# Performance work log

Measured on AMD Instinct MI355X. Metric: run time of the kernel, lower is better.

The kernel has to match this reference:

```python
import jax, jax.numpy as jnp
from jax import lax
import numpy as np


def _dilate3x3(img):
    # Faithful to torch: zero-pad by 1 (f.pad default), then 3x3 max over the
    # padded window (strel of ones => plain max, zeros from padding included).
    imgp = jnp.pad(img, ((0, 0), (0, 0), (1, 1), (1, 1)))
    return lax.reduce_window(imgp, -jnp.inf, lax.max,
                             (1, 1, 3, 3), (1, 1, 1, 1), 'VALID')


def setup_inputs() -> dict:
    key = jax.random.key(0)
    x = jax.random.normal(key, (32, 3, 512, 512), dtype=jnp.float32)
    return {"in_tensor": x, "n_pixels": 20}


def reference(in_tensor, n_pixels):
    # smoother = linspace(1, 0, n+1); smoother_diff = -diff => 1/n per step (linear)
    smoother = jnp.linspace(1.0, 0.0, n_pixels + 1)
    sdiff = (-jnp.diff(smoother)).astype(in_tensor.dtype)  # [n_pixels]

    def step(carry, w):
        out, img = carry
        out = out + w * img
        img = _dilate3x3(img)
        return (out, img), None

    init = (jnp.zeros_like(in_tensor), in_tensor)
    (out, _), _ = lax.scan(step, init, sdiff)
    return out
```

## Files before the change

### kernel.cpp

```cpp
#include <hip/hip_runtime.h>

#define IMG_W 512
#define IMG_H 512
#define TILE 88
#define HALO 20
#define NSTEP 19
#define RH 8
#define RW 8
#define REG 128

__device__ __forceinline__ float max3f(float a, float b, float c) {
    return fmaxf(fmaxf(a, b), c);
}

__device__ __forceinline__ float dpp_shr1(float v) {
    int i = __builtin_bit_cast(int, v);
    i = __builtin_amdgcn_update_dpp(0, i, 0x111, 0xf, 0xf, true);
    return __builtin_bit_cast(float, i);
}
__device__ __forceinline__ float dpp_shl1(float v) {
    int i = __builtin_bit_cast(int, v);
    i = __builtin_amdgcn_update_dpp(0, i, 0x101, 0xf, 0xf, true);
    return __builtin_bit_cast(float, i);
}

__device__ __forceinline__ void hrow(const float (&Ar)[RW], float (&h)[RW]) {
    float hl = dpp_shr1(Ar[RW - 1]);
    float hr = dpp_shl1(Ar[0]);
    h[0] = max3f(hl, Ar[0], Ar[1]);
    #pragma unroll
    for (int c = 1; c < RW - 1; ++c) h[c] = max3f(Ar[c - 1], Ar[c], Ar[c + 1]);
    h[RW - 1] = max3f(Ar[RW - 2], Ar[RW - 1], hr);
}

template<bool XM, bool YM>
__device__ __forceinline__ void rowop(const float (&hm1)[RW], const float (&hc)[RW],
                                      const float (&hn)[RW], float (&Ar)[RW],
                                      float (&accr)[RW], const float (&colm)[RW],
                                      float rm, bool needR) {
    float v[RW];
    #pragma unroll
    for (int c = 0; c < RW; ++c) v[c] = max3f(hm1[c], hc[c], hn[c]);
    if (XM) {
        #pragma unroll
        for (int c = 0; c < RW; ++c) v[c] *= colm[c];
    }
    if (YM) {
        if (needR) {
            #pragma unroll
            for (int c = 0; c < RW; ++c) v[c] *= rm;
        }
    }
    #pragma unroll
    for (int c = 0; c < RW; ++c) { Ar[c] = v[c]; accr[c] += v[c]; }
}

template<bool XM, bool YM>
__device__ __forceinline__ void body(const float* __restrict__ xc, float* __restrict__ oc,
                                     int gx0, int gy0, int tx, int ty,
                                     float4 (*topH4)[2][16][16], float4 (*botH4)[2][16][16]) {
    const int rx = tx * RW;
    const int ry = ty * RH;
    const int gx = gx0 + rx;
    const int gy = gy0 + ry;

    float A[RH][RW];
    float acc[RH][RW];
    float colm[RW], rowm[RH];
    bool needR = false;

    if (XM) {
        #pragma unroll
        for (int c = 0; c < RW; ++c) {
            int xx = gx + c;
            colm[c] = (xx >= 0 && xx < IMG_W) ? 1.f : 0.f;
        }
    }
    if (YM) {
        #pragma unroll
        for (int r = 0; r < RH; ++r) {
            int yy = gy + r;
            rowm[r] = (yy >= 0 && yy < IMG_H) ? 1.f : 0.f;
        }
        needR = (gy < 0) || (gy + RH > IMG_H);
    }

    if (XM || YM) {
        const bool fullin = (gx >= 0) && (gx + RW <= IMG_W) && (gy >= 0) && (gy + RH <= IMG_H);
        if (fullin) {
            #pragma unroll
            for (int r = 0; r < RH; ++r) {
                const float4* rp = (const float4*)(xc + (size_t)(gy + r) * IMG_W + gx);
                float4 v0 = rp[0], v1 = rp[1];
                A[r][0] = v0.x; A[r][1] = v0.y; A[r][2] = v0.z; A[r][3] = v0.w;
                A[r][4] = v1.x; A[r][5] = v1.y; A[r][6] = v1.z; A[r][7] = v1.w;
            }
        } else {
            #pragma unroll
            for (int r = 0; r < RH; ++r) {
                const int yr = gy + r;
                const int yy = min(max(yr, 0), IMG_H - 1);
                float rmv = (yr >= 0 && yr < IMG_H) ? 1.f : 0.f;
                const float* rp = xc + (size_t)yy * IMG_W;
                #pragma unroll
                for (int c = 0; c < RW; ++c) {
                    const int xr = gx + c;
                    const int xx = min(max(xr, 0), IMG_W - 1);
                    float m = rmv;
                    if (XM) m *= colm[c];
                    A[r][c] = rp[xx] * m;
                }
            }
        }
    } else {
        #pragma unroll
        for (int r = 0; r < RH; ++r) {
            const float4* rp = (const float4*)(xc + (size_t)(gy + r) * IMG_W + gx);
            float4 v0 = rp[0], v1 = rp[1];
            A[r][0] = v0.x; A[r][1] = v0.y; A[r][2] = v0.z; A[r][3] = v0.w;
            A[r][4] = v1.x; A[r][5] = v1.y; A[r][6] = v1.z; A[r][7] = v1.w;
        }
    }
    #pragma unroll
    for (int r = 0; r < RH; ++r) {
        #pragma unroll
        for (int c = 0; c < RW; ++c) acc[r][c] = A[r][c];
    }

    #pragma unroll 1
    for (int s = 0; s < NSTEP; ++s) {
        const int buf = s & 1;
        float hc[RW], h7[RW];
        hrow(A[0], hc);
        hrow(A[RH - 1], h7);
        topH4[buf][0][ty][tx] = make_float4(hc[0], hc[1], hc[2], hc[3]);
        topH4[buf][1][ty][tx] = make_float4(hc[4], hc[5], hc[6], hc[7]);
        botH4[buf][0][ty][tx] = make_float4(h7[0], h7[1], h7[2], h7[3]);
        botH4[buf][1][ty][tx] = make_float4(h7[4], h7[5], h7[6], h7[7]);
        __syncthreads();
        const int tyu = ty > 0  ? ty - 1 : 0;
        const int tyd = ty < 15 ? ty + 1 : 15;
        float hm1[RW], hbot[RW];
        {
            float4 u0 = botH4[buf][0][tyu][tx], u1 = botH4[buf][1][tyu][tx];
            float4 d0 = topH4[buf][0][tyd][tx], d1 = topH4[buf][1][tyd][tx];
            hm1[0] = u0.x; hm1[1] = u0.y; hm1[2] = u0.z; hm1[3] = u0.w;
            hm1[4] = u1.x; hm1[5] = u1.y; hm1[6] = u1.z; hm1[7] = u1.w;
            hbot[0] = d0.x; hbot[1] = d0.y; hbot[2] = d0.z; hbot[3] = d0.w;
            hbot[4] = d1.x; hbot[5] = d1.y; hbot[6] = d1.z; hbot[7] = d1.w;
        }
        #pragma unroll
        for (int r = 0; r < RH; ++r) {
            float hn[RW];
            if (r < RH - 2) {
                hrow(A[r + 1], hn);
            } else if (r == RH - 2) {
                #pragma unroll
                for (int c = 0; c < RW; ++c) hn[c] = h7[c];
            } else {
                #pragma unroll
                for (int c = 0; c < RW; ++c) hn[c] = hbot[c];
            }
            rowop<XM, YM>(hm1, hc, hn, A[r], acc[r], colm, YM ? rowm[r] : 1.f, needR);
            #pragma unroll
            for (int c = 0; c < RW; ++c) { hm1[c] = hc[c]; hc[c] = hn[c]; }
        }
    }

    if (XM || YM) {
        #pragma unroll
        for (int r = 0; r < RH; ++r) {
            const int rr = ry + r;
            const int yy = gy0 + rr;
            if (rr >= HALO && rr < HALO + TILE && yy < IMG_H) {
                #pragma unroll
                for (int c = 0; c < RW; ++c) {
                    const int cc = rx + c;
                    const int xx = gx0 + cc;
                    if (cc >= HALO && cc < HALO + TILE && xx < IMG_W)
                        oc[(size_t)yy * IMG_W + xx] = 0.05f * acc[r][c];
                }
            }
        }
    } else {
        #pragma unroll
        for (int r = 0; r < RH; ++r) {
            const int rr = ry + r;
            if (rr < HALO || rr >= HALO + TILE) continue;
            const int yy = gy0 + rr;
            float* rowp = oc + (size_t)yy * IMG_W + gx;
            if (tx >= 3 && tx <= 12) {
                ((float4*)rowp)[0] = make_float4(0.05f * acc[r][0], 0.05f * acc[r][1],
                                                 0.05f * acc[r][2], 0.05f * acc[r][3]);
                ((float4*)rowp)[1] = make_float4(0.05f * acc[r][4], 0.05f * acc[r][5],
                                                 0.05f * acc[r][6], 0.05f * acc[r][7]);
            } else if (tx == 2) {
                ((float4*)rowp)[1] = make_float4(0.05f * acc[r][4], 0.05f * acc[r][5],
                                                 0.05f * acc[r][6], 0.05f * acc[r][7]);
            } else if (tx == 13) {
                ((float4*)rowp)[0] = make_float4(0.05f * acc[r][0], 0.05f * acc[r][1],
                                                 0.05f * acc[r][2], 0.05f * acc[r][3]);
            }
        }
    }
}

__global__ __launch_bounds__(256, 2)
void blur_outwards_kernel(const float* __restrict__ x, float* __restrict__ out) {
    __shared__ float4 topH4[2][2][16][16];
    __shared__ float4 botH4[2][2][16][16];

    const int tid = threadIdx.x;
    const int tx = tid & 15;
    const int ty = tid >> 4;

    const int ch  = blockIdx.z;
    const int gx0 = (int)blockIdx.x * TILE - HALO;
    const int gy0 = (int)blockIdx.y * TILE - HALO;

    const float* __restrict__ xc = x + (size_t)ch * (IMG_W * IMG_H);
    float* __restrict__ oc = out + (size_t)ch * (IMG_W * IMG_H);

    const bool xe = (gx0 < 0) || (gx0 + REG > IMG_W);
    const bool ye = (gy0 < 0) || (gy0 + REG > IMG_H);
    if (!xe && !ye)      body<false, false>(xc, oc, gx0, gy0, tx, ty, topH4, botH4);
    else if (xe && !ye)  body<true,  false>(xc, oc, gx0, gy0, tx, ty, topH4, botH4);
    else if (!xe && ye)  body<false, true >(xc, oc, gx0, gy0, tx, ty, topH4, botH4);
    else                 body<true,  true >(xc, oc, gx0, gy0, tx, ty, topH4, botH4);
}

extern "C" void kernel_launch(void* const* d_in, const int* in_sizes, int n_in,
                              void* d_out, int out_size, void* d_ws, size_t ws_size,
                              hipStream_t stream) {
    const float* x = (const float*)d_in[0];
    float* out = (float*)d_out;
    dim3 grid((IMG_W + TILE - 1) / TILE,
              (IMG_H + TILE - 1) / TILE,
              96);
    blur_outwards_kernel<<<grid, 256, 0, stream>>>(x, out);
}
```

Measured before the change: 313.0 us.

## Software-pipeline halo exchange by updating boundary rows first each step

```diff
diff --git a/kernel.cpp b/kernel.cpp
--- a/kernel.cpp
+++ b/kernel.cpp
@@ -127,43 +127,61 @@
         for (int c = 0; c < RW; ++c) acc[r][c] = A[r][c];
     }
 
+    const int tyu = ty > 0  ? ty - 1 : 0;
+    const int tyd = ty < 15 ? ty + 1 : 15;
+
+    float ht[RW], hb[RW];
+    hrow(A[0], ht); hrow(A[RH - 1], hb);
+    topH4[0][0][ty][tx] = make_float4(ht[0], ht[1], ht[2], ht[3]);
+    topH4[0][1][ty][tx] = make_float4(ht[4], ht[5], ht[6], ht[7]);
+    botH4[0][0][ty][tx] = make_float4(hb[0], hb[1], hb[2], hb[3]);
+    botH4[0][1][ty][tx] = make_float4(hb[4], hb[5], hb[6], hb[7]);
+    __syncthreads();
+    float4 u0 = botH4[0][0][tyu][tx], u1 = botH4[0][1][tyu][tx];
+    float4 d0 = topH4[0][0][tyd][tx], d1 = topH4[0][1][tyd][tx];
+
     #pragma unroll 1
     for (int s = 0; s < NSTEP; ++s) {
-        const int buf = s & 1;
-        float hc[RW], h7[RW];
-        hrow(A[0], hc);
-        hrow(A[RH - 1], h7);
-        topH4[buf][0][ty][tx] = make_float4(hc[0], hc[1], hc[2], hc[3]);
-        topH4[buf][1][ty][tx] = make_float4(hc[4], hc[5], hc[6], hc[7]);
-        botH4[buf][0][ty][tx] = make_float4(h7[0], h7[1], h7[2], h7[3]);
-        botH4[buf][1][ty][tx] = make_float4(h7[4], h7[5], h7[6], h7[7]);
-        __syncthreads();
-        const int tyu = ty > 0  ? ty - 1 : 0;
-        const int tyd = ty < 15 ? ty + 1 : 15;
-        float hm1[RW], hbot[RW];
-        {
-            float4 u0 = botH4[buf][0][tyu][tx], u1 = botH4[buf][1][tyu][tx];
-            float4 d0 = topH4[buf][0][tyd][tx], d1 = topH4[buf][1][tyd][tx];
-            hm1[0] = u0.x; hm1[1] = u0.y; hm1[2] = u0.z; hm1[3] = u0.w;
-            hm1[4] = u1.x; hm1[5] = u1.y; hm1[6] = u1.z; hm1[7] = u1.w;
-            hbot[0] = d0.x; hbot[1] = d0.y; hbot[2] = d0.z; hbot[3] = d0.w;
-            hbot[4] = d1.x; hbot[5] = d1.y; hbot[6] = d1.z; hbot[7] = d1.w;
-        }
-        #pragma unroll
-        for (int r = 0; r < RH; ++r) {
-            float hn[RW];
-            if (r < RH - 2) {
-                hrow(A[r + 1], hn);
-            } else if (r == RH - 2) {
-                #pragma unroll
-                for (int c = 0; c < RW; ++c) hn[c] = h7[c];
-            } else {
-                #pragma unroll
-                for (int c = 0; c < RW; ++c) hn[c] = hbot[c];
-            }
-            rowop<XM, YM>(hm1, hc, hn, A[r], acc[r], colm, YM ? rowm[r] : 1.f, needR);
-            #pragma unroll
-            for (int c = 0; c < RW; ++c) { hm1[c] = hc[c]; hc[c] = hn[c]; }
+        float hm1[RW], hbt[RW];
+        hm1[0] = u0.x; hm1[1] = u0.y; hm1[2] = u0.z; hm1[3] = u0.w;
+        hm1[4] = u1.x; hm1[5] = u1.y; hm1[6] = u1.z; hm1[7] = u1.w;
+        hbt[0] = d0.x; hbt[1] = d0.y; hbt[2] = d0.z; hbt[3] = d0.w;
+        hbt[4] = d1.x; hbt[5] = d1.y; hbt[6] = d1.z; hbt[7] = d1.w;
+
+        float h1[RW]; hrow(A[1], h1);
+        rowop<XM, YM>(hm1, ht, h1, A[0], acc[0], colm, YM ? rowm[0] : 1.f, needR);
+        float h6[RW]; hrow(A[6], h6);
+        rowop<XM, YM>(h6, hb, hbt, A[7], acc[7], colm, YM ? rowm[7] : 1.f, needR);
+
+        const int nbuf = (s & 1) ^ 1;
+        const bool more = (s + 1 < NSTEP);
+        float htn[RW], hbn[RW];
+        if (more) {
+            hrow(A[0], htn);
+            hrow(A[7], hbn);
+            topH4[nbuf][0][ty][tx] = make_float4(htn[0], htn[1], htn[2], htn[3]);
+            topH4[nbuf][1][ty][tx] = make_float4(htn[4], htn[5], htn[6], htn[7]);
+            botH4[nbuf][0][ty][tx] = make_float4(hbn[0], hbn[1], hbn[2], hbn[3]);
+            botH4[nbuf][1][ty][tx] = make_float4(hbn[4], hbn[5], hbn[6], hbn[7]);
+        }
+
+        float h2[RW]; hrow(A[2], h2);
+        rowop<XM, YM>(ht, h1, h2, A[1], acc[1], colm, YM ? rowm[1] : 1.f, needR);
+        float h3[RW]; hrow(A[3], h3);
+        rowop<XM, YM>(h1, h2, h3, A[2], acc[2], colm, YM ? rowm[2] : 1.f, needR);
+        float h4[RW]; hrow(A[4], h4);
+        rowop<XM, YM>(h2, h3, h4, A[3], acc[3], colm, YM ? rowm[3] : 1.f, needR);
+        float h5[RW]; hrow(A[5], h5);
+        rowop<XM, YM>(h3, h4, h5, A[4], acc[4], colm, YM ? rowm[4] : 1.f, needR);
+        rowop<XM, YM>(h4, h5, h6, A[5], acc[5], colm, YM ? rowm[5] : 1.f, needR);
+        rowop<XM, YM>(h5, h6, hb, A[6], acc[6], colm, YM ? rowm[6] : 1.f, needR);
+
+        if (more) {
+            __syncthreads();
+            u0 = botH4[nbuf][0][tyu][tx]; u1 = botH4[nbuf][1][tyu][tx];
+            d0 = topH4[nbuf][0][tyd][tx]; d1 = topH4[nbuf][1][tyd][tx];
+            #pragma unroll
+            for (int c = 0; c < RW; ++c) { ht[c] = htn[c]; hb[c] = hbn[c]; }
         }
     }
 
```

Result: slower. 328.3 us (+4.9%).

## Exchange intra-wave row halos via ds_bpermute, keep LDS only for wave boundaries

Applied to the files above, without the earlier changes.

```diff
diff --git a/kernel.cpp b/kernel.cpp
--- a/kernel.cpp
+++ b/kernel.cpp
@@ -23,6 +23,10 @@
     i = __builtin_amdgcn_update_dpp(0, i, 0x101, 0xf, 0xf, true);
     return __builtin_bit_cast(float, i);
 }
+__device__ __forceinline__ float bperm(int byteAddr, float v) {
+    int i = __builtin_amdgcn_ds_bpermute(byteAddr, __builtin_bit_cast(int, v));
+    return __builtin_bit_cast(float, i);
+}
 
 __device__ __forceinline__ void hrow(const float (&Ar)[RW], float (&h)[RW]) {
     float hl = dpp_shr1(Ar[RW - 1]);
@@ -57,8 +61,8 @@
 
 template<bool XM, bool YM>
 __device__ __forceinline__ void body(const float* __restrict__ xc, float* __restrict__ oc,
-                                     int gx0, int gy0, int tx, int ty,
-                                     float4 (*topH4)[2][16][16], float4 (*botH4)[2][16][16]) {
+                                     int gx0, int gy0, int tx, int ty, int lane,
+                                     float4 (*botR)[4][16][2], float4 (*topR)[4][16][2]) {
     const int rx = tx * RW;
     const int ry = ty * RH;
     const int gx = gx0 + rx;
@@ -127,44 +131,59 @@
         for (int c = 0; c < RW; ++c) acc[r][c] = A[r][c];
     }
 
+    const int upA = ((lane - 16) & 63) << 2;
+    const int dnA = ((lane + 16) & 63) << 2;
+    const int gq = ty >> 2;
+    const int tw = ty & 3;
+
     #pragma unroll 1
     for (int s = 0; s < NSTEP; ++s) {
-        const int buf = s & 1;
         float hc[RW], h7[RW];
         hrow(A[0], hc);
         hrow(A[RH - 1], h7);
-        topH4[buf][0][ty][tx] = make_float4(hc[0], hc[1], hc[2], hc[3]);
-        topH4[buf][1][ty][tx] = make_float4(hc[4], hc[5], hc[6], hc[7]);
-        botH4[buf][0][ty][tx] = make_float4(h7[0], h7[1], h7[2], h7[3]);
-        botH4[buf][1][ty][tx] = make_float4(h7[4], h7[5], h7[6], h7[7]);
+        float hm1[RW], hbot[RW];
+        #pragma unroll
+        for (int c = 0; c < RW; ++c) hm1[c] = bperm(upA, h7[c]);
+        #pragma unroll
+        for (int c = 0; c < RW; ++c) hbot[c] = bperm(dnA, hc[c]);
+
+        const int buf = s & 1;
+        if (tw == 3) {
+            botR[buf][gq][tx][0] = make_float4(h7[0], h7[1], h7[2], h7[3]);
+            botR[buf][gq][tx][1] = make_float4(h7[4], h7[5], h7[6], h7[7]);
+        } else if (tw == 0) {
+            topR[buf][gq][tx][0] = make_float4(hc[0], hc[1], hc[2], hc[3]);
+            topR[buf][gq][tx][1] = make_float4(hc[4], hc[5], hc[6], hc[7]);
+        }
         __syncthreads();
-        const int tyu = ty > 0  ? ty - 1 : 0;
-        const int tyd = ty < 15 ? ty + 1 : 15;
-        float hm1[RW], hbot[RW];
-        {
-            float4 u0 = botH4[buf][0][tyu][tx], u1 = botH4[buf][1][tyu][tx];
-            float4 d0 = topH4[buf][0][tyd][tx], d1 = topH4[buf][1][tyd][tx];
-            hm1[0] = u0.x; hm1[1] = u0.y; hm1[2] = u0.z; hm1[3] = u0.w;
-            hm1[4] = u1.x; hm1[5] = u1.y; hm1[6] = u1.z; hm1[7] = u1.w;
-            hbot[0] = d0.x; hbot[1] = d0.y; hbot[2] = d0.z; hbot[3] = d0.w;
-            hbot[4] = d1.x; hbot[5] = d1.y; hbot[6] = d1.z; hbot[7] = d1.w;
-        }
-        #pragma unroll
-        for (int r = 0; r < RH; ++r) {
-            float hn[RW];
-            if (r < RH - 2) {
-                hrow(A[r + 1], hn);
-            } else if (r == RH - 2) {
-                #pragma unroll
-                for (int c = 0; c < RW; ++c) hn[c] = h7[c];
-            } else {
-                #pragma unroll
-                for (int c = 0; c < RW; ++c) hn[c] = hbot[c];
-            }
-            rowop<XM, YM>(hm1, hc, hn, A[r], acc[r], colm, YM ? rowm[r] : 1.f, needR);
-            #pragma unroll
-            for (int c = 0; c < RW; ++c) { hm1[c] = hc[c]; hc[c] = hn[c]; }
-        }
+        if (tw == 0) {
+            if (gq > 0) {
+                float4 u0 = botR[buf][gq - 1][tx][0], u1 = botR[buf][gq - 1][tx][1];
+                hm1[0] = u0.x; hm1[1] = u0.y; hm1[2] = u0.z; hm1[3] = u0.w;
+                hm1[4] = u1.x; hm1[5] = u1.y; hm1[6] = u1.z; hm1[7] = u1.w;
+            }
+        } else if (tw == 3) {
+            if (gq < 3) {
+                float4 d0 = topR[buf][gq + 1][tx][0], d1 = topR[buf][gq + 1][tx][1];
+                hbot[0] = d0.x; hbot[1] = d0.y; hbot[2] = d0.z; hbot[3] = d0.w;
+                hbot[4] = d1.x; hbot[5] = d1.y; hbot[6] = d1.z; hbot[7] = d1.w;
+            }
+        }
+
+        float h1[RW]; hrow(A[1], h1);
+        float h2[RW]; hrow(A[2], h2);
+        rowop<XM, YM>(hc, h1, h2, A[1], acc[1], colm, YM ? rowm[1] : 1.f, needR);
+        rowop<XM, YM>(hm1, hc, h1, A[0], acc[0], colm, YM ? rowm[0] : 1.f, needR);
+        float h3[RW]; hrow(A[3], h3);
+        rowop<XM, YM>(h1, h2, h3, A[2], acc[2], colm, YM ? rowm[2] : 1.f, needR);
+        float h4[RW]; hrow(A[4], h4);
+        rowop<XM, YM>(h2, h3, h4, A[3], acc[3], colm, YM ? rowm[3] : 1.f, needR);
+        float h5[RW]; hrow(A[5], h5);
+        rowop<XM, YM>(h3, h4, h5, A[4], acc[4], colm, YM ? rowm[4] : 1.f, needR);
+        float h6[RW]; hrow(A[6], h6);
+        rowop<XM, YM>(h4, h5, h6, A[5], acc[5], colm, YM ? rowm[5] : 1.f, needR);
+        rowop<XM, YM>(h5, h6, h7, A[6], acc[6], colm, YM ? rowm[6] : 1.f, needR);
+        rowop<XM, YM>(h6, h7, hbot, A[7], acc[7], colm, YM ? rowm[7] : 1.f, needR);
     }
 
     if (XM || YM) {
@@ -207,12 +226,13 @@
 
 __global__ __launch_bounds__(256, 2)
 void blur_outwards_kernel(const float* __restrict__ x, float* __restrict__ out) {
-    __shared__ float4 topH4[2][2][16][16];
-    __shared__ float4 botH4[2][2][16][16];
+    __shared__ float4 botR[2][4][16][2];
+    __shared__ float4 topR[2][4][16][2];
 
     const int tid = threadIdx.x;
     const int tx = tid & 15;
     const int ty = tid >> 4;
+    const int lane = tid & 63;
 
     const int ch  = blockIdx.z;
     const int gx0 = (int)blockIdx.x * TILE - HALO;
@@ -223,10 +243,10 @@
 
     const bool xe = (gx0 < 0) || (gx0 + REG > IMG_W);
     const bool ye = (gy0 < 0) || (gy0 + REG > IMG_H);
-    if (!xe && !ye)      body<false, false>(xc, oc, gx0, gy0, tx, ty, topH4, botH4);
-    else if (xe && !ye)  body<true,  false>(xc, oc, gx0, gy0, tx, ty, topH4, botH4);
-    else if (!xe && ye)  body<false, true >(xc, oc, gx0, gy0, tx, ty, topH4, botH4);
-    else                 body<true,  true >(xc, oc, gx0, gy0, tx, ty, topH4, botH4);
+    if (!xe && !ye)      body<false, false>(xc, oc, gx0, gy0, tx, ty, lane, botR, topR);
+    else if (xe && !ye)  body<true,  false>(xc, oc, gx0, gy0, tx, ty, lane, botR, topR);
+    else if (!xe && ye)  body<false, true >(xc, oc, gx0, gy0, tx, ty, lane, botR, topR);
+    else                 body<true,  true >(xc, oc, gx0, gy0, tx, ty, lane, botR, topR);
 }
 
 extern "C" void kernel_launch(void* const* d_in, const int* in_sizes, int n_in,
```

New measurement: 313.9 us. No clear change (+0.3%).

## Halve per-thread rows to 4 and double block to 512 threads

Applied to the files above, without the earlier changes.

```diff
diff --git a/kernel.cpp b/kernel.cpp
--- a/kernel.cpp
+++ b/kernel.cpp
@@ -5,7 +5,7 @@
 #define TILE 88
 #define HALO 20
 #define NSTEP 19
-#define RH 8
+#define RH 4
 #define RW 8
 #define REG 128
 
@@ -58,7 +58,7 @@
 template<bool XM, bool YM>
 __device__ __forceinline__ void body(const float* __restrict__ xc, float* __restrict__ oc,
                                      int gx0, int gy0, int tx, int ty,
-                                     float4 (*topH4)[2][16][16], float4 (*botH4)[2][16][16]) {
+                                     float4 (*topH4)[2][32][16], float4 (*botH4)[2][32][16]) {
     const int rx = tx * RW;
     const int ry = ty * RH;
     const int gx = gx0 + rx;
@@ -127,19 +127,20 @@
         for (int c = 0; c < RW; ++c) acc[r][c] = A[r][c];
     }
 
+    const int tyu = ty > 0  ? ty - 1 : 0;
+    const int tyd = ty < 31 ? ty + 1 : 31;
+
     #pragma unroll 1
     for (int s = 0; s < NSTEP; ++s) {
         const int buf = s & 1;
-        float hc[RW], h7[RW];
-        hrow(A[0], hc);
-        hrow(A[RH - 1], h7);
-        topH4[buf][0][ty][tx] = make_float4(hc[0], hc[1], hc[2], hc[3]);
-        topH4[buf][1][ty][tx] = make_float4(hc[4], hc[5], hc[6], hc[7]);
-        botH4[buf][0][ty][tx] = make_float4(h7[0], h7[1], h7[2], h7[3]);
-        botH4[buf][1][ty][tx] = make_float4(h7[4], h7[5], h7[6], h7[7]);
+        float h0[RW], h3[RW];
+        hrow(A[0], h0);
+        hrow(A[RH - 1], h3);
+        topH4[buf][0][ty][tx] = make_float4(h0[0], h0[1], h0[2], h0[3]);
+        topH4[buf][1][ty][tx] = make_float4(h0[4], h0[5], h0[6], h0[7]);
+        botH4[buf][0][ty][tx] = make_float4(h3[0], h3[1], h3[2], h3[3]);
+        botH4[buf][1][ty][tx] = make_float4(h3[4], h3[5], h3[6], h3[7]);
         __syncthreads();
-        const int tyu = ty > 0  ? ty - 1 : 0;
-        const int tyd = ty < 15 ? ty + 1 : 15;
         float hm1[RW], hbot[RW];
         {
             float4 u0 = botH4[buf][0][tyu][tx], u1 = botH4[buf][1][tyu][tx];
@@ -149,22 +150,12 @@
             hbot[0] = d0.x; hbot[1] = d0.y; hbot[2] = d0.z; hbot[3] = d0.w;
             hbot[4] = d1.x; hbot[5] = d1.y; hbot[6] = d1.z; hbot[7] = d1.w;
         }
-        #pragma unroll
-        for (int r = 0; r < RH; ++r) {
-            float hn[RW];
-            if (r < RH - 2) {
-                hrow(A[r + 1], hn);
-            } else if (r == RH - 2) {
-                #pragma unroll
-                for (int c = 0; c < RW; ++c) hn[c] = h7[c];
-            } else {
-                #pragma unroll
-                for (int c = 0; c < RW; ++c) hn[c] = hbot[c];
-            }
-            rowop<XM, YM>(hm1, hc, hn, A[r], acc[r], colm, YM ? rowm[r] : 1.f, needR);
-            #pragma unroll
-            for (int c = 0; c < RW; ++c) { hm1[c] = hc[c]; hc[c] = hn[c]; }
-        }
+        float h1[RW]; hrow(A[1], h1);
+        rowop<XM, YM>(hm1, h0, h1, A[0], acc[0], colm, YM ? rowm[0] : 1.f, needR);
+        float h2[RW]; hrow(A[2], h2);
+        rowop<XM, YM>(h0, h1, h2, A[1], acc[1], colm, YM ? rowm[1] : 1.f, needR);
+        rowop<XM, YM>(h1, h2, h3, A[2], acc[2], colm, YM ? rowm[2] : 1.f, needR);
+        rowop<XM, YM>(h2, h3, hbot, A[3], acc[3], colm, YM ? rowm[3] : 1.f, needR);
     }
 
     if (XM || YM) {
@@ -183,32 +174,32 @@
             }
         }
     } else {
-        #pragma unroll
-        for (int r = 0; r < RH; ++r) {
-            const int rr = ry + r;
-            if (rr < HALO || rr >= HALO + TILE) continue;
-            const int yy = gy0 + rr;
-            float* rowp = oc + (size_t)yy * IMG_W + gx;
-            if (tx >= 3 && tx <= 12) {
-                ((float4*)rowp)[0] = make_float4(0.05f * acc[r][0], 0.05f * acc[r][1],
-                                                 0.05f * acc[r][2], 0.05f * acc[r][3]);
-                ((float4*)rowp)[1] = make_float4(0.05f * acc[r][4], 0.05f * acc[r][5],
-                                                 0.05f * acc[r][6], 0.05f * acc[r][7]);
-            } else if (tx == 2) {
-                ((float4*)rowp)[1] = make_float4(0.05f * acc[r][4], 0.05f * acc[r][5],
-                                                 0.05f * acc[r][6], 0.05f * acc[r][7]);
-            } else if (tx == 13) {
-                ((float4*)rowp)[0] = make_float4(0.05f * acc[r][0], 0.05f * acc[r][1],
-                                                 0.05f * acc[r][2], 0.05f * acc[r][3]);
-            }
-        }
-    }
-}
-
-__global__ __launch_bounds__(256, 2)
+        if (ty >= 5 && ty <= 26) {
+            #pragma unroll
+            for (int r = 0; r < RH; ++r) {
+                const int yy = gy0 + ry + r;
+                float* rowp = oc + (size_t)yy * IMG_W + gx;
+                if (tx >= 3 && tx <= 12) {
+                    ((float4*)rowp)[0] = make_float4(0.05f * acc[r][0], 0.05f * acc[r][1],
+                                                     0.05f * acc[r][2], 0.05f * acc[r][3]);
+                    ((float4*)rowp)[1] = make_float4(0.05f * acc[r][4], 0.05f * acc[r][5],
+                                                     0.05f * acc[r][6], 0.05f * acc[r][7]);
+                } else if (tx == 2) {
+                    ((float4*)rowp)[1] = make_float4(0.05f * acc[r][4], 0.05f * acc[r][5],
+                                                     0.05f * acc[r][6], 0.05f * acc[r][7]);
+                } else if (tx == 13) {
+                    ((float4*)rowp)[0] = make_float4(0.05f * acc[r][0], 0.05f * acc[r][1],
+                                                     0.05f * acc[r][2], 0.05f * acc[r][3]);
+                }
+            }
+        }
+    }
+}
+
+__global__ __launch_bounds__(512, 4)
 void blur_outwards_kernel(const float* __restrict__ x, float* __restrict__ out) {
-    __shared__ float4 topH4[2][2][16][16];
-    __shared__ float4 botH4[2][2][16][16];
+    __shared__ float4 topH4[2][2][32][16];
+    __shared__ float4 botH4[2][2][32][16];
 
     const int tid = threadIdx.x;
     const int tx = tid & 15;
@@ -237,5 +228,5 @@
     dim3 grid((IMG_W + TILE - 1) / TILE,
               (IMG_H + TILE - 1) / TILE,
               96);
-    blur_outwards_kernel<<<grid, 256, 0, stream>>>(x, out);
-}
+    blur_outwards_kernel<<<grid, 512, 0, stream>>>(x, out);
+}
```

Result: faster. 302.6 us (-3.3%).
